# Kernel tuning notes

Hardware: AMD Instinct MI355X
Metric: run time of the kernel (lower is better)

The kernel has to match this reference:

```python
import jax, jax.numpy as jnp
import numpy as np

B, IN_DIM, OUT_DIM, N = 8, 128, 128, 256
BN_EPS = 1e-5


def setup_inputs() -> dict:
    key = jax.random.key(0)
    ks = jax.random.split(key, 6)
    A = jax.random.normal(ks[0], (B, IN_DIM, N), dtype=jnp.float32)
    ini_p = float(np.sqrt(3.0 / OUT_DIM / IN_DIM))
    ini_qk = float(np.sqrt(1.0 / OUT_DIM / IN_DIM))
    P1 = jax.random.uniform(ks[1], (OUT_DIM, IN_DIM), minval=-ini_p, maxval=ini_p, dtype=jnp.float32)
    P2 = jax.random.uniform(ks[2], (OUT_DIM, IN_DIM), minval=-ini_p, maxval=ini_p, dtype=jnp.float32)
    q = jax.random.uniform(ks[3], (OUT_DIM, IN_DIM), minval=-ini_qk, maxval=ini_qk, dtype=jnp.float32)
    k = jax.random.uniform(ks[4], (OUT_DIM, IN_DIM), minval=-ini_qk, maxval=ini_qk, dtype=jnp.float32)
    gamma = jnp.ones((OUT_DIM,), dtype=jnp.float32)
    beta = jnp.zeros((OUT_DIM,), dtype=jnp.float32)
    return {"A": A, "P1": P1, "P2": P2, "q": q, "k": k,
            "gamma": gamma, "beta": beta,
            "permutation_size1": N, "BATCH_SIZE": B}


def reference(A, P1, P2, q, k, gamma, beta, permutation_size1, BATCH_SIZE):
    # A: [B, in_dim, n]; params [out_dim, in_dim]
    A1 = jnp.einsum('oi,bin->bon', P1, A)            # [B, C, n]
    Q = jnp.einsum('oi,bin->bon', q, A)              # [B, C, n]
    K = jnp.einsum('oi,bin->bon', k, A)              # [B, C, n]
    # Rank-1 outer product per (b, c): Alpha[b,c,i,j] = Q[b,c,i] * K[b,c,j]
    Alpha = Q[..., :, None] * K[..., None, :]        # [B, C, n, n]
    row_norm = jnp.linalg.norm(Alpha, axis=3, keepdims=True)  # [B, C, n, 1]
    Alpha_norm = jnp.abs(Alpha) / row_norm
    V = jnp.einsum('oi,bin->bon', P2, A)             # [B, C, n]
    Y = jnp.einsum('bcij,bcj->bci', Alpha_norm, V)   # [B, C, n]
    out = A1 + V + 0.1 * Y
    out = jax.nn.relu(out)
    # BatchNorm1d (training mode): normalize per channel over (B, n)
    mean = out.mean(axis=(0, 2), keepdims=True)
    var = out.var(axis=(0, 2), keepdims=True)
    out = (out - mean) * jax.lax.rsqrt(var + BN_EPS)
    out = out * gamma[None, :, None] + beta[None, :, None]
    return out
```

## Files before the change

kernel.cpp:

```cpp
#include <hip/hip_runtime.h>
#include <math.h>

#define BB   8
#define IND  128
#define OUTD 128
#define NN   256
#define NQ   64
#define BN_EPS 1e-5f

__global__ __launch_bounds__(64) void k1_proj(
    const float* __restrict__ A,
    const float* __restrict__ P1,
    const float* __restrict__ P2,
    const float* __restrict__ kw,
    float* __restrict__ pbuf,
    float* __restrict__ bnp)
{
    const int c = blockIdx.x;
    const int b = blockIdx.y;
    const int x = threadIdx.x;

    const float4* __restrict__ A4 = (const float4*)A + (size_t)b * IND * NQ;
    const float* __restrict__ w1 = P1 + c * IND;
    const float* __restrict__ w2 = P2 + c * IND;
    const float* __restrict__ w3 = kw + c * IND;

    float a1[4] = {0.f, 0.f, 0.f, 0.f};
    float vv[4] = {0.f, 0.f, 0.f, 0.f};
    float kv[4] = {0.f, 0.f, 0.f, 0.f};

    #pragma unroll
    for (int blk = 0; blk < 16; ++blk) {
        float4 cur[8];
        #pragma unroll
        for (int j = 0; j < 8; ++j)
            cur[j] = A4[(blk * 8 + j) * NQ + x];
        #pragma unroll
        for (int j = 0; j < 8; ++j) {
            const int i = blk * 8 + j;
            const float wa = w1[i], wb = w2[i], wc = w3[i];
            a1[0] = fmaf(wa, cur[j].x, a1[0]); a1[1] = fmaf(wa, cur[j].y, a1[1]);
            a1[2] = fmaf(wa, cur[j].z, a1[2]); a1[3] = fmaf(wa, cur[j].w, a1[3]);
            vv[0] = fmaf(wb, cur[j].x, vv[0]); vv[1] = fmaf(wb, cur[j].y, vv[1]);
            vv[2] = fmaf(wb, cur[j].z, vv[2]); vv[3] = fmaf(wb, cur[j].w, vv[3]);
            kv[0] = fmaf(wc, cur[j].x, kv[0]); kv[1] = fmaf(wc, cur[j].y, kv[1]);
            kv[2] = fmaf(wc, cur[j].z, kv[2]); kv[3] = fmaf(wc, cur[j].w, kv[3]);
        }
    }

    float s2 = 0.f, sv = 0.f;
    #pragma unroll
    for (int j = 0; j < 4; ++j) {
        s2 = fmaf(kv[j], kv[j], s2);
        sv = fmaf(fabsf(kv[j]), vv[j], sv);
    }
    #pragma unroll
    for (int off = 32; off >= 1; off >>= 1) {
        s2 += __shfl_xor(s2, off, 64);
        sv += __shfl_xor(sv, off, 64);
    }
    const float y = sv / sqrtf(s2);

    float p[4];
    float bnsum = 0.f, bnsq = 0.f;
    #pragma unroll
    for (int j = 0; j < 4; ++j) {
        float t = a1[j] + vv[j] + 0.1f * y;
        t = fmaxf(t, 0.f);
        p[j] = t;
        bnsum += t;
        bnsq  = fmaf(t, t, bnsq);
    }
    #pragma unroll
    for (int off = 32; off >= 1; off >>= 1) {
        bnsum += __shfl_xor(bnsum, off, 64);
        bnsq  += __shfl_xor(bnsq,  off, 64);
    }

    float4* __restrict__ p4 = (float4*)pbuf;
    p4[((size_t)b * OUTD + c) * NQ + x] = make_float4(p[0], p[1], p[2], p[3]);
    if (x == 0) {
        bnp[c * BB + b]              = bnsum;
        bnp[OUTD * BB + c * BB + b]  = bnsq;
    }
}

__global__ __launch_bounds__(512) void k2_bn(
    const float* __restrict__ pbuf,
    const float* __restrict__ bnp,
    const float* __restrict__ gamma,
    const float* __restrict__ beta,
    float* __restrict__ out)
{
    const int c = blockIdx.x;
    const int x = threadIdx.x;
    const int b = threadIdx.y;

    float tsum = 0.f, tsq = 0.f;
    #pragma unroll
    for (int w = 0; w < BB; ++w) {
        tsum += bnp[c * BB + w];
        tsq  += bnp[OUTD * BB + c * BB + w];
    }
    const float inv   = 1.f / (float)(BB * NN);
    const float mean  = tsum * inv;
    const float var   = tsq * inv - mean * mean;
    const float scale = gamma[c] * rsqrtf(var + BN_EPS);
    const float shift = beta[c] - mean * scale;

    const float4* __restrict__ p4 = (const float4*)pbuf;
    float4* __restrict__ out4 = (float4*)out;
    const size_t idx = ((size_t)b * OUTD + c) * NQ + x;
    const float4 p = p4[idx];
    out4[idx] = make_float4(fmaf(p.x, scale, shift), fmaf(p.y, scale, shift),
                            fmaf(p.z, scale, shift), fmaf(p.w, scale, shift));
}

extern "C" void kernel_launch(void* const* d_in, const int* in_sizes, int n_in,
                              void* d_out, int out_size, void* d_ws, size_t ws_size,
                              hipStream_t stream) {
    const float* A     = (const float*)d_in[0];
    const float* P1    = (const float*)d_in[1];
    const float* P2    = (const float*)d_in[2];
    const float* kw    = (const float*)d_in[4];
    const float* gamma = (const float*)d_in[5];
    const float* beta  = (const float*)d_in[6];
    float* out = (float*)d_out;

    float* pbuf = (float*)d_ws;
    float* bnp  = (float*)((char*)d_ws + (size_t)BB * OUTD * NN * sizeof(float));

    dim3 g1(OUTD, BB);
    k1_proj<<<g1, 64, 0, stream>>>(A, P1, P2, kw, pbuf, bnp);
    dim3 b2(64, BB);
    k2_bn<<<OUTD, b2, 0, stream>>>(pbuf, bnp, gamma, beta, out);
}
```

Measured before the change: 77.88 us.

## Fuse projection and batch-norm kernels via cooperative grid sync

Merges the projection kernel and the BN-apply kernel into one cooperative kernel. Post-ReLU values stay in registers across a grid-wide barrier instead of being written to and reread from an intermediate buffer. This removes one kernel launch and a full round trip of the activation tensor through global memory. In exchange it adds the cost of a grid sync and needs all 1024 single-wave blocks to be co-resident.

```diff
diff --git a/kernel.cpp b/kernel.cpp
--- a/kernel.cpp
+++ b/kernel.cpp
@@ -1,5 +1,8 @@
 #include <hip/hip_runtime.h>
+#include <hip/hip_cooperative_groups.h>
 #include <math.h>
+
+namespace cg = cooperative_groups;
 
 #define BB   8
 #define IND  128
@@ -8,13 +11,15 @@
 #define NQ   64
 #define BN_EPS 1e-5f
 
-__global__ __launch_bounds__(64) void k1_proj(
+__global__ __launch_bounds__(64) void layer1dpe_coop(
     const float* __restrict__ A,
     const float* __restrict__ P1,
     const float* __restrict__ P2,
     const float* __restrict__ kw,
-    float* __restrict__ pbuf,
-    float* __restrict__ bnp)
+    const float* __restrict__ gamma,
+    const float* __restrict__ beta,
+    float* __restrict__ bnp,
+    float* __restrict__ out)
 {
     const int c = blockIdx.x;
     const int b = blockIdx.y;
@@ -76,25 +81,12 @@
         bnsum += __shfl_xor(bnsum, off, 64);
         bnsq  += __shfl_xor(bnsq,  off, 64);
     }
+    if (x == 0) {
+        bnp[c * BB + b]             = bnsum;
+        bnp[OUTD * BB + c * BB + b] = bnsq;
+    }
 
-    float4* __restrict__ p4 = (float4*)pbuf;
-    p4[((size_t)b * OUTD + c) * NQ + x] = make_float4(p[0], p[1], p[2], p[3]);
-    if (x == 0) {
-        bnp[c * BB + b]              = bnsum;
-        bnp[OUTD * BB + c * BB + b]  = bnsq;
-    }
-}
-
-__global__ __launch_bounds__(512) void k2_bn(
-    const float* __restrict__ pbuf,
-    const float* __restrict__ bnp,
-    const float* __restrict__ gamma,
-    const float* __restrict__ beta,
-    float* __restrict__ out)
-{
-    const int c = blockIdx.x;
-    const int x = threadIdx.x;
-    const int b = threadIdx.y;
+    cg::this_grid().sync();
 
     float tsum = 0.f, tsq = 0.f;
     #pragma unroll
@@ -108,12 +100,10 @@
     const float scale = gamma[c] * rsqrtf(var + BN_EPS);
     const float shift = beta[c] - mean * scale;
 
-    const float4* __restrict__ p4 = (const float4*)pbuf;
     float4* __restrict__ out4 = (float4*)out;
-    const size_t idx = ((size_t)b * OUTD + c) * NQ + x;
-    const float4 p = p4[idx];
-    out4[idx] = make_float4(fmaf(p.x, scale, shift), fmaf(p.y, scale, shift),
-                            fmaf(p.z, scale, shift), fmaf(p.w, scale, shift));
+    out4[((size_t)b * OUTD + c) * NQ + x] = make_float4(
+        fmaf(p[0], scale, shift), fmaf(p[1], scale, shift),
+        fmaf(p[2], scale, shift), fmaf(p[3], scale, shift));
 }
 
 extern "C" void kernel_launch(void* const* d_in, const int* in_sizes, int n_in,
@@ -125,13 +115,12 @@
     const float* kw    = (const float*)d_in[4];
     const float* gamma = (const float*)d_in[5];
     const float* beta  = (const float*)d_in[6];
-    float* out = (float*)d_out;
+    float* out  = (float*)d_out;
+    float* bnp  = (float*)d_ws;
 
-    float* pbuf = (float*)d_ws;
-    float* bnp  = (float*)((char*)d_ws + (size_t)BB * OUTD * NN * sizeof(float));
-
-    dim3 g1(OUTD, BB);
-    k1_proj<<<g1, 64, 0, stream>>>(A, P1, P2, kw, pbuf, bnp);
-    dim3 b2(64, BB);
-    k2_bn<<<OUTD, b2, 0, stream>>>(pbuf, bnp, gamma, beta, out);
+    void* args[] = { (void*)&A, (void*)&P1, (void*)&P2, (void*)&kw,
+                     (void*)&gamma, (void*)&beta, (void*)&bnp, (void*)&out };
+    dim3 grid(OUTD, BB);
+    dim3 block(64);
+    hipLaunchCooperativeKernel((void*)layer1dpe_coop, grid, block, args, 0, stream);
 }
```

Measured after the change: 142.7 us. +83.3%, slower.
